# Kernel optimization log

Hardware: AMD Instinct MI355X
Metric: run time of the kernel (lower is better)

The kernel has to match this reference:

```python
import jax, jax.numpy as jnp
import numpy as np

NUM_SEQS = 4
SEQ_LEN = 2048
T = NUM_SEQS * SEQ_LEN          # total tokens
D_IN = 4096
D_OUT = 4096
NUM_ADAPTERS = 8
MAX_RANK = 64
CACHE_LEN = NUM_ADAPTERS * MAX_RANK  # 512 pages


def setup_inputs() -> dict:
    key = jax.random.key(0)
    ks = jax.random.split(key, 8)
    x = jax.random.normal(ks[0], (T, D_IN), dtype=jnp.float32)
    weight = jax.random.normal(ks[1], (D_OUT, D_IN), dtype=jnp.float32) * 0.02
    bias = jax.random.normal(ks[2], (D_OUT,), dtype=jnp.float32) * 0.02
    a_cache = jax.random.normal(ks[3], (CACHE_LEN, D_IN), dtype=jnp.float32) * 0.02
    b_cache = jax.random.normal(ks[4], (CACHE_LEN, D_OUT), dtype=jnp.float32) * 0.02
    b_start_loc = (jnp.arange(NUM_SEQS) * SEQ_LEN).astype(jnp.int32)
    b_adapter_ids = jax.random.randint(ks[5], (NUM_SEQS,), 0, NUM_ADAPTERS).astype(jnp.int32)
    b_scaling = jax.random.uniform(ks[6], (NUM_SEQS,), dtype=jnp.float32, minval=0.5, maxval=2.0)
    # page i for (adapter a, rank slot r) lives at a*MAX_RANK + r
    rank_page_table = jnp.arange(CACHE_LEN, dtype=jnp.int32).reshape(NUM_ADAPTERS, MAX_RANK)
    ranks = jax.random.randint(ks[7], (NUM_ADAPTERS,), 1, MAX_RANK + 1).astype(jnp.int32)
    return {"x": x, "weight": weight, "bias": bias, "a_cache": a_cache,
            "b_cache": b_cache, "b_start_loc": b_start_loc,
            "b_adapter_ids": b_adapter_ids, "b_scaling": b_scaling,
            "rank_page_table": rank_page_table, "ranks": ranks}


def reference(x, weight, bias, a_cache, b_cache, b_start_loc,
              b_adapter_ids, b_scaling, rank_page_table, ranks):
    t = x.shape[0]
    num_adapters, max_rank = rank_page_table.shape
    # map each token to its sequence -> adapter id / scaling (mbgmm dispatch)
    seg = jnp.searchsorted(b_start_loc, jnp.arange(t, dtype=b_start_loc.dtype),
                           side='right') - 1                      # [T]
    tok_adapter = b_adapter_ids[seg]                              # [T]
    tok_scale = b_scaling[seg]                                    # [T]
    # gather paged LoRA A/B weights per adapter: [A, R, D]
    A_all = a_cache[rank_page_table]                              # [A, R, D_in]
    B_all = b_cache[rank_page_table]                              # [A, R, D_out]
    # mbgmm_a: xa[t, r] = x[t] . A[adapter(t), r], zero beyond rank
    xa_all = jnp.einsum('td,ard->tar', x, A_all)                  # [T, A, R]
    rmask = (jnp.arange(max_rank)[None, :] < ranks[:, None])      # [A, R]
    onehot = (tok_adapter[:, None] == jnp.arange(num_adapters)[None, :])  # [T, A]
    sel = (onehot[:, :, None] & rmask[None, :, :]).astype(x.dtype)  # [T, A, R]
    xa_sel = xa_all * sel
    # mbgmm_b: lora_out[t] = scaling * sum_r xa[t, r] * B[adapter(t), r]
    lora_out = jnp.einsum('tar,aro->to', xa_sel, B_all) * tok_scale[:, None]
    base_out = x @ weight.T + bias
    return base_out + lora_out
```

## Files before the change

### kernel.cpp

```cpp
#include <hip/hip_runtime.h>
#include <hip/hip_bf16.h>

typedef unsigned short u16;
typedef unsigned int u32;
typedef __attribute__((ext_vector_type(8))) short bf16x8;
typedef __attribute__((ext_vector_type(4))) float f32x4;

#define T_TOK 8192
#define DIN 4096
#define DOUT 4096
#define N_SEQS 4
#define N_ADPT 8
#define MAXR 64
#define CACHE_LEN 512

__device__ __forceinline__ u16 f2bf(float f) {
    u32 u = __builtin_bit_cast(u32, f);
    u += 0x7fffu + ((u >> 16) & 1u);
    return (u16)(u >> 16);
}

__device__ __forceinline__ void load_lds16(const u16* g, u16* l) {
    __builtin_amdgcn_global_load_lds(
        (const __attribute__((address_space(1))) u32*)g,
        (__attribute__((address_space(3))) u32*)l, 16, 0, 0);
}

__global__ void cvt_kernel(const float* __restrict__ in, u16* __restrict__ out, int n4) {
    int i = blockIdx.x * blockDim.x + threadIdx.x;
    int stride = gridDim.x * blockDim.x;
    for (; i < n4; i += stride) {
        float4 v = reinterpret_cast<const float4*>(in)[i];
        ushort4 o;
        o.x = f2bf(v.x); o.y = f2bf(v.y); o.z = f2bf(v.z); o.w = f2bf(v.w);
        reinterpret_cast<ushort4*>(out)[i] = o;
    }
}

__global__ void build_bt(const float* __restrict__ b_cache, const int* __restrict__ rpt,
                         u16* __restrict__ Bt) {
    int id = blockIdx.x * 256 + threadIdx.x;
    int n  = id & (DOUT - 1);
    int rb = (id >> 12) & 7;
    int a  = id >> 15;
    union { u16 u[8]; uint4 v; } pack;
    #pragma unroll
    for (int j = 0; j < 8; ++j) {
        int r = rb * 8 + j;
        int page = rpt[a * MAXR + r];
        pack.u[j] = f2bf(b_cache[(long)page * DOUT + n]);
    }
    *reinterpret_cast<uint4*>(&Bt[((long)(a * DOUT + n)) * MAXR + rb * 8]) = pack.v;
}

__launch_bounds__(256)
__global__ void xa_kernel(const u16* __restrict__ xb, const u16* __restrict__ ab,
                          const int* __restrict__ b_start_loc,
                          const int* __restrict__ b_adapter_ids,
                          const float* __restrict__ b_scaling,
                          const int* __restrict__ rpt,
                          const int* __restrict__ ranks,
                          u16* __restrict__ xa) {
    int t0 = blockIdx.x * 128;
    int seg = 0;
    #pragma unroll
    for (int i = 1; i < N_SEQS; ++i) if (b_start_loc[i] <= t0) seg = i;
    int adapter = b_adapter_ids[seg];
    float scale = b_scaling[seg];
    int rank = ranks[adapter];

    __shared__ __attribute__((aligned(16))) u16 As[128 * 32];
    __shared__ __attribute__((aligned(16))) u16 Bs[64 * 32];

    int tid = threadIdx.x;
    int lane = tid & 63, wave = tid >> 6;
    int lr = lane & 15, lk = lane >> 4;

    int e0 = wave * 64 + lane;
    int e1 = 256 + e0;
    int ra0 = e0 >> 2, ca0 = (e0 & 3) * 8;
    int ra1 = e1 >> 2, ca1 = (e1 & 3) * 8;
    const u16* gA0 = xb + (long)(t0 + ra0) * DIN + ca0;
    const u16* gA1 = xb + (long)(t0 + ra1) * DIN + ca1;
    int rB = ra0;
    int page = rpt[adapter * MAXR + rB];
    const u16* gB = ab + (long)page * DIN + ca0;

    f32x4 acc[2][4] = {};

    for (int k0 = 0; k0 < DIN; k0 += 32) {
        load_lds16(gA0 + k0, As + wave * 512);
        load_lds16(gA1 + k0, As + 2048 + wave * 512);
        load_lds16(gB + k0,  Bs + wave * 512);
        asm volatile("s_waitcnt vmcnt(0)" ::: "memory");
        __syncthreads();
        bf16x8 af[2], bfr[4];
        #pragma unroll
        for (int m = 0; m < 2; ++m)
            af[m] = *(const bf16x8*)&As[(wave * 32 + m * 16 + lr) * 32 + lk * 8];
        #pragma unroll
        for (int n = 0; n < 4; ++n)
            bfr[n] = *(const bf16x8*)&Bs[(n * 16 + lr) * 32 + lk * 8];
        #pragma unroll
        for (int m = 0; m < 2; ++m)
            #pragma unroll
            for (int n = 0; n < 4; ++n)
                acc[m][n] = __builtin_amdgcn_mfma_f32_16x16x32_bf16(af[m], bfr[n], acc[m][n], 0, 0, 0);
        __syncthreads();
    }

    #pragma unroll
    for (int m = 0; m < 2; ++m) {
        int trow = t0 + wave * 32 + m * 16 + lk * 4;
        #pragma unroll
        for (int n = 0; n < 4; ++n) {
            int r = n * 16 + lr;
            #pragma unroll
            for (int j = 0; j < 4; ++j) {
                float v = (r < rank) ? acc[m][n][j] * scale : 0.0f;
                xa[(long)(trow + j) * MAXR + r] = f2bf(v);
            }
        }
    }
}

__launch_bounds__(512, 2)
__global__ void gemm256_kernel(const u16* __restrict__ xb, const u16* __restrict__ wb,
                               const float* __restrict__ bias,
                               const u16* __restrict__ xa, const u16* __restrict__ Bt,
                               const int* __restrict__ b_start_loc,
                               const int* __restrict__ b_adapter_ids,
                               float* __restrict__ out) {
    __shared__ __attribute__((aligned(16))) u16 lds[32768];

    int bid = blockIdx.x;
    int wgid = (bid & 7) * 64 + (bid >> 3);
    int mt = wgid >> 4, nt = wgid & 15;
    int brow = mt * 256, bcol = nt * 256;

    int seg = 0;
    #pragma unroll
    for (int i = 1; i < N_SEQS; ++i) if (b_start_loc[i] <= brow) seg = i;
    int adapter = b_adapter_ids[seg];

    int tid = threadIdx.x;
    int lane = tid & 63, wave = tid >> 6;
    int wm = wave >> 2, wn = wave & 3;
    int lr = lane & 15, lk = lane >> 4;

    int lsw = (tid & 7) ^ ((tid >> 3) & 7);
    int c8  = (lsw & 3) * 8;
    int r0  = (tid >> 3) * 2 + (lsw >> 2);
    const long odA0 = (long)(brow + r0) * DIN + c8;
    const long odA1 = odA0 + 128L * DIN;
    const long odB0 = (long)(bcol + r0) * DIN + c8;
    const long odB1 = odB0 + 128L * DIN;
    const long o6A0 = (long)(brow + r0) * MAXR + c8;
    const long o6A1 = o6A0 + 128L * MAXR;
    const long o6B0 = (long)(adapter * DOUT + bcol + r0) * MAXR + c8;
    const long o6B1 = o6B0 + 128L * MAXR;

    #define STAGE(T, buf)                                                          \
        do {                                                                       \
            u16* dA = lds + (buf) * 8192 + tid * 8;                                \
            u16* dB = lds + 16384 + (buf) * 8192 + tid * 8;                        \
            if ((T) < 128) {                                                       \
                long ko = (long)(T) * 32;                                          \
                load_lds16(xb + odA0 + ko, dA);                                    \
                load_lds16(xb + odA1 + ko, dA + 4096);                             \
                load_lds16(wb + odB0 + ko, dB);                                    \
                load_lds16(wb + odB1 + ko, dB + 4096);                             \
            } else {                                                               \
                long ko = (long)((T) - 128) * 32;                                  \
                load_lds16(xa + o6A0 + ko, dA);                                    \
                load_lds16(xa + o6A1 + ko, dA + 4096);                             \
                load_lds16(Bt + o6B0 + ko, dB);                                    \
                load_lds16(Bt + o6B1 + ko, dB + 4096);                             \
            }                                                                      \
        } while (0)

    const int laneByte = (lr >> 1) * 128 + 16 * ((((lr & 1) << 2) + lk) ^ (lr >> 1));
    const char* ldsc = (const char*)lds;
    const int cA = wm * 8192 + laneByte;
    const int cB = 32768 + wn * 4096 + laneByte;

    f32x4 acc[8][4] = {};

    STAGE(0, 0);

    for (int t = 0; t < 130; ++t) {
        const int b = t & 1;
        if (t < 129) {
            STAGE(t + 1, b ^ 1);
            asm volatile("s_waitcnt vmcnt(4)" ::: "memory");
        } else {
            asm volatile("s_waitcnt vmcnt(0)" ::: "memory");
        }
        __builtin_amdgcn_s_barrier();
        __builtin_amdgcn_sched_barrier(0);

        const char* pA = ldsc + b * 16384 + cA;
        const char* pB = ldsc + b * 16384 + cB;

        bf16x8 bfr[4], af[8];
        #pragma unroll
        for (int ni = 0; ni < 4; ++ni)
            bfr[ni] = *(const bf16x8*)(pB + ni * 1024);
        #pragma unroll
        for (int mi = 0; mi < 8; ++mi)
            af[mi] = *(const bf16x8*)(pA + mi * 1024);

        __builtin_amdgcn_s_setprio(1);
        #pragma unroll
        for (int mi = 0; mi < 8; ++mi)
            #pragma unroll
            for (int ni = 0; ni < 4; ++ni)
                acc[mi][ni] = __builtin_amdgcn_mfma_f32_16x16x32_bf16(
                    af[mi], bfr[ni], acc[mi][ni], 0, 0, 0);
        __builtin_amdgcn_s_setprio(0);

        if (t < 129) {
            __builtin_amdgcn_s_barrier();
            __builtin_amdgcn_sched_barrier(0);
        }
    }
    #undef STAGE

    #pragma unroll
    for (int m = 0; m < 8; ++m) {
        int orow = brow + wm * 128 + m * 16 + lk * 4;
        #pragma unroll
        for (int n = 0; n < 4; ++n) {
            int ocol = bcol + wn * 64 + n * 16 + lr;
            float bv = bias[ocol];
            #pragma unroll
            for (int j = 0; j < 4; ++j)
                out[(long)(orow + j) * DOUT + ocol] = acc[m][n][j] + bv;
        }
    }
}

extern "C" void kernel_launch(void* const* d_in, const int* in_sizes, int n_in,
                              void* d_out, int out_size, void* d_ws, size_t ws_size,
                              hipStream_t stream) {
    const float* x          = (const float*)d_in[0];
    const float* weight     = (const float*)d_in[1];
    const float* bias       = (const float*)d_in[2];
    const float* a_cache    = (const float*)d_in[3];
    const float* b_cache    = (const float*)d_in[4];
    const int*   b_start    = (const int*)d_in[5];
    const int*   b_adapter  = (const int*)d_in[6];
    const float* b_scaling  = (const float*)d_in[7];
    const int*   rpt        = (const int*)d_in[8];
    const int*   ranks      = (const int*)d_in[9];
    float* out = (float*)d_out;

    char* ws = (char*)d_ws;
    u16* xb = (u16*)ws; ws += (size_t)T_TOK * DIN * 2;
    u16* wb = (u16*)ws; ws += (size_t)DOUT * DIN * 2;
    u16* ab = (u16*)ws; ws += (size_t)CACHE_LEN * DIN * 2;
    u16* Bt = (u16*)ws; ws += (size_t)N_ADPT * DOUT * MAXR * 2;
    u16* xa = (u16*)ws; ws += (size_t)T_TOK * MAXR * 2;

    cvt_kernel<<<2048, 256, 0, stream>>>(x, xb, T_TOK * DIN / 4);
    cvt_kernel<<<2048, 256, 0, stream>>>(weight, wb, DOUT * DIN / 4);
    cvt_kernel<<<512, 256, 0, stream>>>(a_cache, ab, CACHE_LEN * DIN / 4);
    build_bt<<<(N_ADPT * 8 * DOUT) / 256, 256, 0, stream>>>(b_cache, rpt, Bt);
    xa_kernel<<<T_TOK / 128, 256, 0, stream>>>(xb, ab, b_start, b_adapter, b_scaling, rpt, ranks, xa);
    gemm256_kernel<<<(T_TOK / 256) * (DOUT / 256), 512, 0, stream>>>(xb, wb, bias, xa, Bt, b_start, b_adapter, out);
}
```

Measured before the change: 371.5 us.

## Double-buffer LDS fragment reads in registers to overlap with MFMA

Restructures the main GEMM loop into a two-step unrolled pipeline. Each step reads the next tile's A/B fragments from LDS into a second register set while MFMAs run on the previously loaded fragments. This hides LDS read latency behind matrix math. The cost is extra VGPRs for the duplicate fragment buffers, and the tail iterations issue redundant clamped STAGE loads.

```diff
diff --git a/kernel.cpp b/kernel.cpp
--- a/kernel.cpp
+++ b/kernel.cpp
@@ -184,47 +184,66 @@
     const int cA = wm * 8192 + laneByte;
     const int cB = 32768 + wn * 4096 + laneByte;
 
+    #define READF(FA, FB, par)                                                     \
+        do {                                                                       \
+            const char* pA = ldsc + (par) * 16384 + cA;                            \
+            const char* pB = ldsc + (par) * 16384 + cB;                            \
+            _Pragma("unroll")                                                      \
+            for (int ni = 0; ni < 4; ++ni) FB[ni] = *(const bf16x8*)(pB + ni * 1024); \
+            _Pragma("unroll")                                                      \
+            for (int mi = 0; mi < 8; ++mi) FA[mi] = *(const bf16x8*)(pA + mi * 1024); \
+        } while (0)
+
+    #define MFMA32(FA, FB)                                                         \
+        do {                                                                       \
+            __builtin_amdgcn_s_setprio(1);                                         \
+            _Pragma("unroll")                                                      \
+            for (int mi = 0; mi < 8; ++mi)                                         \
+                _Pragma("unroll")                                                  \
+                for (int ni = 0; ni < 4; ++ni)                                     \
+                    acc[mi][ni] = __builtin_amdgcn_mfma_f32_16x16x32_bf16(         \
+                        FA[mi], FB[ni], acc[mi][ni], 0, 0, 0);                     \
+            __builtin_amdgcn_s_setprio(0);                                         \
+        } while (0)
+
+    #define ENDBAR()                                                               \
+        do {                                                                       \
+            asm volatile("s_waitcnt lgkmcnt(0)" ::: "memory");                     \
+            __builtin_amdgcn_sched_barrier(0);                                     \
+            __builtin_amdgcn_s_barrier();                                          \
+        } while (0)
+
     f32x4 acc[8][4] = {};
+    bf16x8 fA0[8], fB0[4], fA1[8], fB1[4];
 
     STAGE(0, 0);
-
-    for (int t = 0; t < 130; ++t) {
-        const int b = t & 1;
-        if (t < 129) {
-            STAGE(t + 1, b ^ 1);
-            asm volatile("s_waitcnt vmcnt(4)" ::: "memory");
-        } else {
-            asm volatile("s_waitcnt vmcnt(0)" ::: "memory");
-        }
+    STAGE(1, 1);
+    asm volatile("s_waitcnt vmcnt(4)" ::: "memory");
+    __builtin_amdgcn_s_barrier();
+    READF(fA0, fB0, 0);
+    ENDBAR();
+
+    for (int t = 0; t < 130; t += 2) {
+        STAGE((t + 2 < 130) ? t + 2 : 129, t & 1);
+        asm volatile("s_waitcnt vmcnt(4)" ::: "memory");
         __builtin_amdgcn_s_barrier();
-        __builtin_amdgcn_sched_barrier(0);
-
-        const char* pA = ldsc + b * 16384 + cA;
-        const char* pB = ldsc + b * 16384 + cB;
-
-        bf16x8 bfr[4], af[8];
-        #pragma unroll
-        for (int ni = 0; ni < 4; ++ni)
-            bfr[ni] = *(const bf16x8*)(pB + ni * 1024);
-        #pragma unroll
-        for (int mi = 0; mi < 8; ++mi)
-            af[mi] = *(const bf16x8*)(pA + mi * 1024);
-
-        __builtin_amdgcn_s_setprio(1);
-        #pragma unroll
-        for (int mi = 0; mi < 8; ++mi)
-            #pragma unroll
-            for (int ni = 0; ni < 4; ++ni)
-                acc[mi][ni] = __builtin_amdgcn_mfma_f32_16x16x32_bf16(
-                    af[mi], bfr[ni], acc[mi][ni], 0, 0, 0);
-        __builtin_amdgcn_s_setprio(0);
-
-        if (t < 129) {
-            __builtin_amdgcn_s_barrier();
-            __builtin_amdgcn_sched_barrier(0);
-        }
-    }
+        READF(fA1, fB1, (t + 1) & 1);
+        MFMA32(fA0, fB0);
+        ENDBAR();
+
+        STAGE((t + 3 < 130) ? t + 3 : 129, (t + 1) & 1);
+        asm volatile("s_waitcnt vmcnt(4)" ::: "memory");
+        __builtin_amdgcn_s_barrier();
+        if (t + 2 < 130) READF(fA0, fB0, t & 1);
+        MFMA32(fA1, fB1);
+        ENDBAR();
+    }
+    asm volatile("s_waitcnt vmcnt(0)" ::: "memory");
+
     #undef STAGE
+    #undef READF
+    #undef MFMA32
+    #undef ENDBAR
 
     #pragma unroll
     for (int m = 0; m < 8; ++m) {
```

New measurement: 366.9 us. No clear change (-1.2%).
